# Performance work log

Hardware: AMD Instinct MI355X
Metric: run time of the kernel (lower is better)

## Reference

```python
import jax, jax.numpy as jnp
import numpy as np

TEMP = 0.07  # init temperature
EPS = 1e-12  # F.normalize eps


def _per_cloud_loss(fmap, labels):
    # fmap: [C, N] per-point features; labels: [N] int
    v = fmap.T  # [N, C]
    v = v / jnp.maximum(jnp.linalg.norm(v, axis=1, keepdims=True), EPS)
    # NxN similarity, exp then divide by temp (order matches original)
    dot = jnp.exp(v @ v.T) / TEMP  # [N, N]
    dot = dot - jnp.diag(jnp.diag(dot))  # zero the diagonal
    mask = (labels[:, None] == labels[None, :]).astype(dot.dtype)  # [N, N]
    mask_not = 1.0 - mask
    pos = (mask * dot).sum(1) / mask.sum(1)  # note: denom includes self, as in original
    neg = (mask_not * dot).sum(1) / mask_not.sum(1)
    return jnp.mean(-jnp.log(pos / (pos + neg)))


def setup_inputs() -> dict:
    key = jax.random.key(0)
    k1, k2 = jax.random.split(key)
    B, C, N = 8, 128, 4096
    features = jax.random.normal(k1, (B, C, N), dtype=jnp.float32)
    labels_all = jax.random.randint(k2, (B, N), 0, 16, dtype=jnp.int64)
    return {"features": features, "labels_all": labels_all}


def reference(features, labels_all):
    losses = jax.vmap(_per_cloud_loss)(features, labels_all)  # [B]
    return jnp.mean(losses)
```

## Files before the change

### kernel.cpp

```cpp
#include <hip/hip_runtime.h>
#include <stdint.h>

#define NPTS 4096
#define NC 128
#define NB 8
#define CSPLIT 8
#define COLS_PER (NPTS / CSPLIT)
#define TILES (COLS_PER / 64)
#define RPB 256

typedef __bf16 bf16x8 __attribute__((ext_vector_type(8)));
typedef float f32x4 __attribute__((ext_vector_type(4)));
typedef unsigned short u16;
typedef unsigned int u32;
typedef unsigned long long u64;

__device__ inline float fast_exp2(float x) { return __builtin_amdgcn_exp2f(x); }

__device__ inline u16 f2bf(float x) {
    u32 u = __float_as_uint(x);
    u32 r = (u + 0x7fffu + ((u >> 16) & 1u)) >> 16;
    return (u16)r;
}

typedef __attribute__((address_space(1))) const void glb_void;
typedef __attribute__((address_space(3))) void lds_void;
__device__ inline void gload_lds16(const void* g, void* l) {
    __builtin_amdgcn_global_load_lds((glb_void*)g, (lds_void*)l, 16, 0, 0);
}

__device__ inline bf16x8 scale8(bf16x8 v) {
#pragma unroll
    for (int k = 0; k < 8; ++k) v[k] = (__bf16)((float)v[k] * 1.44269504f);
    return v;
}

__global__ __launch_bounds__(256) void hist_kernel(const int* __restrict__ labels,
                                                   int* __restrict__ counts,
                                                   int* __restrict__ baseg,
                                                   u32* __restrict__ zb) {
    int b = blockIdx.x, tid = threadIdx.x;
    if (b == 0 && tid < 2) zb[tid] = 0u;
    __shared__ int cnt[64][16];
    __shared__ int tot[16];
    for (int i = tid; i < 64 * 16; i += 256) ((int*)cnt)[i] = 0;
    __syncthreads();
    for (int n = tid; n < NPTS; n += 256)
        atomicAdd(&cnt[n >> 6][labels[b * NPTS + n] & 15], 1);
    __syncthreads();
    if (tid < 16) {
        int s = 0;
        for (int k = 0; k < 64; ++k) s += cnt[k][tid];
        counts[b * 16 + tid] = s;
        tot[tid] = s;
    }
    __syncthreads();
    if (tid == 0) {
        int run = 0;
        for (int l = 0; l < 16; ++l) { int c = tot[l]; tot[l] = run; run += c; }
    }
    __syncthreads();
    if (tid < 16) {
        int run = tot[tid];
        for (int k = 0; k < 64; ++k) {
            baseg[(b * 64 + k) * 16 + tid] = run;
            run += cnt[k][tid];
        }
    }
}

__global__ __launch_bounds__(256) void norm_kernel(const float* __restrict__ feat,
                                                   const int* __restrict__ labels,
                                                   const int* __restrict__ baseg,
                                                   u16* __restrict__ vbf,
                                                   int* __restrict__ slab) {
    int b = blockIdx.y;
    int blk = blockIdx.x;
    int tid = threadIdx.x;
    int n0 = blk * 64;
    __shared__ float tile[64][129];
    __shared__ float part[8][64];
    __shared__ float rn[64];
    __shared__ int lpos[64];
    const float* fb = feat + (size_t)b * NC * NPTS;
    int nslot = tid & 31;
    int ty = tid >> 5;
    float s0 = 0.f, s1 = 0.f;
#pragma unroll
    for (int i = 0; i < 16; ++i) {
        int c = i * 8 + ty;
        float2 x = *(const float2*)(fb + (size_t)c * NPTS + n0 + 2 * nslot);
        tile[2 * nslot][c] = x.x;
        tile[2 * nslot + 1][c] = x.y;
        s0 += x.x * x.x;
        s1 += x.y * x.y;
    }
    part[ty][2 * nslot] = s0;
    part[ty][2 * nslot + 1] = s1;
    __syncthreads();
    if (tid < 64) {
        float s = 0.f;
#pragma unroll
        for (int t = 0; t < 8; ++t) s += part[t][tid];
        rn[tid] = 1.f / fmaxf(sqrtf(s), 1e-12f);
        int myl = labels[b * NPTS + n0 + tid] & 15;
        u64 mymask = 0ull;
#pragma unroll
        for (int L = 0; L < 16; ++L) {
            u64 bl = __ballot(myl == L);
            if (myl == L) mymask = bl;
        }
        int rank = __popcll(mymask & ((1ull << tid) - 1ull));
        int pos = baseg[(b * 64 + blk) * 16 + myl] + rank;
        lpos[tid] = pos;
        slab[b * NPTS + pos] = myl;
    }
    __syncthreads();
    u32* out = (u32*)vbf;
#pragma unroll
    for (int i = 0; i < 16; ++i) {
        int idx = tid + i * 256;
        int p = idx >> 6, k = idx & 63;
        float r = rn[p];
        float x0 = tile[p][2 * k] * r;
        float x1 = tile[p][2 * k + 1] * r;
        out[((size_t)b * NPTS + lpos[p]) * 64 + k] = (u32)f2bf(x0) | ((u32)f2bf(x1) << 16);
    }
}


#define META(S)                                                                   \
    const int rbase##S = row0 + wave * 64 + S * 16;                               \
    const int lrp##S = lab[rbase##S + myq] | (lab[rbase##S + myq + 1] << 8) |     \
                       (lab[rbase##S + myq + 2] << 16) |                          \
                       (lab[rbase##S + myq + 3] << 24);                           \
    const int slo##S = __builtin_amdgcn_readfirstlane(lab[rbase##S]);             \
    const int shi##S = __builtin_amdgcn_readfirstlane(lab[rbase##S + 15]);        \
    const bool suni##S = (slo##S == shi##S);                                      \
    const int key##S =                                                            \
        __builtin_amdgcn_readfirstlane((rbase##S & ~63) | ((rbase##S >> 4) & 3));

#define LDA(S)                                                                    \
    bf16x8 af##S##0, af##S##1, af##S##2, af##S##3;                                \
    {                                                                             \
        const u16* ap = vb + (size_t)(rbase##S + ln) * NC + quad * 8;             \
        af##S##0 = scale8(*(const bf16x8*)(ap));                                  \
        af##S##1 = scale8(*(const bf16x8*)(ap + 32));                             \
        af##S##2 = scale8(*(const bf16x8*)(ap + 64));                             \
        af##S##3 = scale8(*(const bf16x8*)(ap + 96));                             \
    }

#define ACC_MASK(S, L)                                                            \
    {                                                                             \
        bool m0 = (((lrp##S) & 255) == (L));                                      \
        bool m1 = ((((lrp##S) >> 8) & 255) == (L));                               \
        bool m2 = ((((lrp##S) >> 16) & 255) == (L));                              \
        bool m3 = ((((lrp##S) >> 24) & 255) == (L));                              \
        float e0 = fast_exp2(d[0]), e1 = fast_exp2(d[1]);                         \
        float e2 = fast_exp2(d[2]), e3 = fast_exp2(d[3]);                         \
        ps##S[0] += m0 ? e0 : 0.f; pn##S[0] += m0 ? 0.f : e0;                     \
        ps##S[1] += m1 ? e1 : 0.f; pn##S[1] += m1 ? 0.f : e1;                     \
        ps##S[2] += m2 ? e2 : 0.f; pn##S[2] += m2 ? 0.f : e2;                     \
        ps##S[3] += m3 ? e3 : 0.f; pn##S[3] += m3 ? 0.f : e3;                     \
    }

#define DO_S(S)                                                                   \
    {                                                                             \
        f32x4 d = {0.f, 0.f, 0.f, 0.f};                                           \
        d = __builtin_amdgcn_mfma_f32_16x16x32_bf16(af##S##0, bf0, d, 0, 0, 0);   \
        d = __builtin_amdgcn_mfma_f32_16x16x32_bf16(af##S##1, bf1, d, 0, 0, 0);   \
        d = __builtin_amdgcn_mfma_f32_16x16x32_bf16(af##S##2, bf2, d, 0, 0, 0);   \
        d = __builtin_amdgcn_mfma_f32_16x16x32_bf16(af##S##3, bf3, d, 0, 0, 0);   \
        if (key##S == ctsub) {         \
            int lc = clabs[cbase + ln];                                           \
            float e0 = fast_exp2(d[0]), e1 = fast_exp2(d[1]);                     \
            float e2 = fast_exp2(d[2]), e3 = fast_exp2(d[3]);                     \
            if (ln == myq + 0) e0 = 0.f;                                          \
            if (ln == myq + 1) e1 = 0.f;                                          \
            if (ln == myq + 2) e2 = 0.f;                                          \
            if (ln == myq + 3) e3 = 0.f;                                          \
            bool m0 = (((lrp##S) & 255) == lc);                                   \
            bool m1 = ((((lrp##S) >> 8) & 255) == lc);                            \
            bool m2 = ((((lrp##S) >> 16) & 255) == lc);                           \
            bool m3 = ((((lrp##S) >> 24) & 255) == lc);                           \
            ps##S[0] += m0 ? e0 : 0.f; pn##S[0] += m0 ? 0.f : e0;                 \
            ps##S[1] += m1 ? e1 : 0.f; pn##S[1] += m1 ? 0.f : e1;                 \
            ps##S[2] += m2 ? e2 : 0.f; pn##S[2] += m2 ? 0.f : e2;                 \
            ps##S[3] += m3 ? e3 : 0.f; pn##S[3] += m3 ? 0.f : e3;                 \
        } else if (cuni) {                           \
            if (clo < slo##S || clo > shi##S) {          \
                pn##S[0] += fast_exp2(d[0]); pn##S[1] += fast_exp2(d[1]);         \
                pn##S[2] += fast_exp2(d[2]); pn##S[3] += fast_exp2(d[3]);         \
            } else if (suni##S) {                        \
                ps##S[0] += fast_exp2(d[0]); ps##S[1] += fast_exp2(d[1]);         \
                ps##S[2] += fast_exp2(d[2]); ps##S[3] += fast_exp2(d[3]);         \
            } else {             \
                ACC_MASK(S, clo)                                                  \
            }                                                                     \
        } else {                                     \
            int lc2 = clabs[cbase + ln];                                          \
            ACC_MASK(S, lc2)                                                      \
        }                                                                         \
    }

#define STAGE(dst, tt)                                                            \
    gload_lds16(src + (tt) * 1024 + g40, (dst) + (wave * 4 + 0) * 512);           \
    gload_lds16(src + (tt) * 1024 + g41, (dst) + (wave * 4 + 1) * 512);           \
    gload_lds16(src + (tt) * 1024 + g42, (dst) + (wave * 4 + 2) * 512);           \
    gload_lds16(src + (tt) * 1024 + g43, (dst) + (wave * 4 + 3) * 512);

#define RED4(v)                                                                   \
    v[0] += __shfl_xor(v[0], off); v[1] += __shfl_xor(v[1], off);                 \
    v[2] += __shfl_xor(v[2], off); v[3] += __shfl_xor(v[3], off);

#define WR(S)                                                                     \
    {                                                                             \
        size_t o = ((size_t)cs * NB + b) * NPTS + rbase##S + myq;                 \
        float4 w0 = make_float4(ps##S[0], pn##S[0], ps##S[1], pn##S[1]);          \
        float4 w1 = make_float4(ps##S[2], pn##S[2], ps##S[3], pn##S[3]);          \
        *(float4*)(rowacc + 2 * o) = w0;                                          \
        *(float4*)(rowacc + 2 * o + 4) = w1;                                      \
    }

__global__ __launch_bounds__(256, 1) void sim_kernel(const u16* __restrict__ vbf,
                                                     const int* __restrict__ slab,
                                                     float* __restrict__ rowacc) {
    int bid = blockIdx.x;
    int rt = bid >> 6;
    int combo = bid & 63;
    int b = combo >> 3;
    int cs = combo & 7;
    int row0 = rt * RPB;
    int c0 = cs * COLS_PER;
    int tid = threadIdx.x;
    int wave = tid >> 6, lane = tid & 63;
    int quad = lane >> 4, ln = lane & 15;
    int myq = quad * 4;

    const u16* vb = vbf + (size_t)b * NPTS * NC;
    const int* lab = slab + b * NPTS;

    META(0) META(1) META(2) META(3)
    LDA(0) LDA(1) LDA(2) LDA(3)

    f32x4 ps0 = {0.f, 0.f, 0.f, 0.f}, ps1 = ps0, ps2 = ps0, ps3 = ps0;
    f32x4 pn0 = ps0, pn1 = ps0, pn2 = ps0, pn3 = ps0;

    __shared__ u16 cols[2][64 * 128];
    __shared__ int clabs[COLS_PER];
    clabs[tid] = lab[c0 + tid];
    clabs[tid + 256] = lab[c0 + 256 + tid];

    const uint4* src = (const uint4*)(vb + (size_t)c0 * NC);
    const int i160 = (wave * 4 + 0) * 64 + lane;
    const int i161 = (wave * 4 + 1) * 64 + lane;
    const int i162 = (wave * 4 + 2) * 64 + lane;
    const int i163 = (wave * 4 + 3) * 64 + lane;
    const int g40 = (i160 >> 4) * 16 + ((i160 & 15) ^ ((i160 >> 4) & 15));
    const int g41 = (i161 >> 4) * 16 + ((i161 & 15) ^ ((i161 >> 4) & 15));
    const int g42 = (i162 >> 4) * 16 + ((i162 & 15) ^ ((i162 >> 4) & 15));
    const int g43 = (i163 >> 4) * 16 + ((i163 & 15) ^ ((i163 >> 4) & 15));
    const int boff0 = ((0 * 4 + quad) ^ ln) * 8;
    const int boff1 = ((1 * 4 + quad) ^ ln) * 8;
    const int boff2 = ((2 * 4 + quad) ^ ln) * 8;
    const int boff3 = ((3 * 4 + quad) ^ ln) * 8;

    u16* bufA = &cols[0][0];
    u16* bufB = &cols[1][0];

    STAGE(bufA, 0)

    int ct = c0;
    for (int t = 0; t < TILES; ++t, ct += 64) {
        __syncthreads();
        if (t < TILES - 1) { STAGE(bufB, t + 1) }

#pragma unroll
        for (int sub = 0; sub < 4; ++sub) {
            const u16* rowb = bufA + (sub * 16 + ln) * 128;
            bf16x8 bf0 = *(const bf16x8*)(rowb + boff0);
            bf16x8 bf1 = *(const bf16x8*)(rowb + boff1);
            bf16x8 bf2 = *(const bf16x8*)(rowb + boff2);
            bf16x8 bf3 = *(const bf16x8*)(rowb + boff3);
            int cbase = t * 64 + sub * 16;
            int clo = __builtin_amdgcn_readfirstlane(clabs[cbase]);
            int chi = __builtin_amdgcn_readfirstlane(clabs[cbase + 15]);
            bool cuni = (clo == chi);
            int ctsub = ct | sub;
            DO_S(0) DO_S(1) DO_S(2) DO_S(3)
        }
        u16* tmp = bufA; bufA = bufB; bufB = tmp;
    }

#pragma unroll
    for (int off = 1; off < 16; off <<= 1) {
        RED4(ps0) RED4(pn0) RED4(ps1) RED4(pn1)
        RED4(ps2) RED4(pn2) RED4(ps3) RED4(pn3)
    }
    if (ln == 0) { WR(0) WR(1) WR(2) WR(3) }
}

__global__ __launch_bounds__(256) void loss_kernel(const float2* __restrict__ rowacc,
                                                   const int* __restrict__ slab,
                                                   const int* __restrict__ counts,
                                                   float* __restrict__ acc,
                                                   u32* __restrict__ ticket,
                                                   float* __restrict__ out) {
    int idx = blockIdx.x * 256 + threadIdx.x;
    int b = idx >> 12;
    float ps = 0.f, pn = 0.f;
#pragma unroll
    for (int cs = 0; cs < CSPLIT; ++cs) {
        float2 v = rowacc[(size_t)cs * NB * NPTS + idx];
        ps += v.x;
        pn += v.y;
    }
    int lb = slab[idx] & 15;
    int cnt = counts[b * 16 + lb];
    float p = ps / (float)cnt;
    float n = pn / (float)(NPTS - cnt);
    float loss = -__logf(p / (p + n));
#pragma unroll
    for (int off = 1; off < 64; off <<= 1) loss += __shfl_xor(loss, off);
    __shared__ float w[4];
    if ((threadIdx.x & 63) == 0) w[threadIdx.x >> 6] = loss;
    __syncthreads();
    if (threadIdx.x == 0) {
        atomicAdd(acc, w[0] + w[1] + w[2] + w[3]);
        __threadfence();
        u32 t = atomicAdd(ticket, 1u);
        if (t == gridDim.x - 1) {
            float v2 = atomicAdd(acc, 0.f);
            out[0] = v2 * (1.f / (float)(NB * NPTS));
        }
    }
}

extern "C" void kernel_launch(void* const* d_in, const int* in_sizes, int n_in,
                              void* d_out, int out_size, void* d_ws, size_t ws_size,
                              hipStream_t stream) {
    const float* feat = (const float*)d_in[0];
    const int* labels = (const int*)d_in[1];
    float* out = (float*)d_out;

    float* acc = (float*)d_ws;
    u32* ticket = (u32*)((char*)d_ws + 4);
    int* counts = (int*)((char*)d_ws + 256);
    int* baseg = (int*)((char*)d_ws + 1024);
    int* slab = (int*)((char*)d_ws + 36864);
    float* rowacc = (float*)((char*)d_ws + 172032);
    u16* vbf = (u16*)((char*)d_ws + 172032 + (size_t)CSPLIT * NB * NPTS * 8);

    hist_kernel<<<dim3(NB), 256, 0, stream>>>(labels, counts, baseg, (u32*)d_ws);
    norm_kernel<<<dim3(64, NB), 256, 0, stream>>>(feat, labels, baseg, vbf, slab);
    sim_kernel<<<dim3(16 * 64), 256, 0, stream>>>(vbf, slab, rowacc);
    loss_kernel<<<dim3(NB * NPTS / 256), 256, 0, stream>>>((const float2*)rowacc, slab, counts,
                                                           acc, ticket, out);
}
```

Baseline: 141.6 us.

## Load column fragments directly from global into registers, dropping LDS staging

Replaces the double-buffered LDS staging of 64-column tiles (global_load_lds plus per-tile barriers) with direct per-wave global loads of the 16-column B fragments into registers, software-prefetched one group ahead. The diagonal key is simplified to compare against the 16-column group start. This removes __syncthreads and LDS traffic from the loop but makes each wave fetch the column data independently through L1/L2, so global load volume rises fourfold and latency hiding relies on a single group of prefetch.

```diff
diff --git a/kernel.cpp b/kernel.cpp
--- a/kernel.cpp
+++ b/kernel.cpp
@@ -6,7 +6,7 @@
 #define NB 8
 #define CSPLIT 8
 #define COLS_PER (NPTS / CSPLIT)
-#define TILES (COLS_PER / 64)
+#define NGRP (COLS_PER / 16)
 #define RPB 256
 
 typedef __bf16 bf16x8 __attribute__((ext_vector_type(8)));
@@ -21,12 +21,6 @@
     u32 u = __float_as_uint(x);
     u32 r = (u + 0x7fffu + ((u >> 16) & 1u)) >> 16;
     return (u16)r;
-}
-
-typedef __attribute__((address_space(1))) const void glb_void;
-typedef __attribute__((address_space(3))) void lds_void;
-__device__ inline void gload_lds16(const void* g, void* l) {
-    __builtin_amdgcn_global_load_lds((glb_void*)g, (lds_void*)l, 16, 0, 0);
 }
 
 __device__ inline bf16x8 scale8(bf16x8 v) {
@@ -137,8 +131,7 @@
     const int slo##S = __builtin_amdgcn_readfirstlane(lab[rbase##S]);             \
     const int shi##S = __builtin_amdgcn_readfirstlane(lab[rbase##S + 15]);        \
     const bool suni##S = (slo##S == shi##S);                                      \
-    const int key##S =                                                            \
-        __builtin_amdgcn_readfirstlane((rbase##S & ~63) | ((rbase##S >> 4) & 3));
+    const int key##S = __builtin_amdgcn_readfirstlane(rbase##S);
 
 #define LDA(S)                                                                    \
     bf16x8 af##S##0, af##S##1, af##S##2, af##S##3;                                \
@@ -171,7 +164,7 @@
         d = __builtin_amdgcn_mfma_f32_16x16x32_bf16(af##S##1, bf1, d, 0, 0, 0);   \
         d = __builtin_amdgcn_mfma_f32_16x16x32_bf16(af##S##2, bf2, d, 0, 0, 0);   \
         d = __builtin_amdgcn_mfma_f32_16x16x32_bf16(af##S##3, bf3, d, 0, 0, 0);   \
-        if (key##S == ctsub) {         \
+        if (key##S == cg16) {    \
             int lc = clabs[cbase + ln];                                           \
             float e0 = fast_exp2(d[0]), e1 = fast_exp2(d[1]);                     \
             float e2 = fast_exp2(d[2]), e3 = fast_exp2(d[3]);                     \
@@ -187,7 +180,7 @@
             ps##S[1] += m1 ? e1 : 0.f; pn##S[1] += m1 ? 0.f : e1;                 \
             ps##S[2] += m2 ? e2 : 0.f; pn##S[2] += m2 ? 0.f : e2;                 \
             ps##S[3] += m3 ? e3 : 0.f; pn##S[3] += m3 ? 0.f : e3;                 \
-        } else if (cuni) {                           \
+        } else if (cuni) {                          \
             if (clo < slo##S || clo > shi##S) {          \
                 pn##S[0] += fast_exp2(d[0]); pn##S[1] += fast_exp2(d[1]);         \
                 pn##S[2] += fast_exp2(d[2]); pn##S[3] += fast_exp2(d[3]);         \
@@ -197,17 +190,28 @@
             } else {             \
                 ACC_MASK(S, clo)                                                  \
             }                                                                     \
-        } else {                                     \
+        } else {                                    \
             int lc2 = clabs[cbase + ln];                                          \
             ACC_MASK(S, lc2)                                                      \
         }                                                                         \
     }
 
-#define STAGE(dst, tt)                                                            \
-    gload_lds16(src + (tt) * 1024 + g40, (dst) + (wave * 4 + 0) * 512);           \
-    gload_lds16(src + (tt) * 1024 + g41, (dst) + (wave * 4 + 1) * 512);           \
-    gload_lds16(src + (tt) * 1024 + g42, (dst) + (wave * 4 + 2) * 512);           \
-    gload_lds16(src + (tt) * 1024 + g43, (dst) + (wave * 4 + 3) * 512);
+#define PREFETCH()                                                                \
+    nb0 = *(const bf16x8*)(bp);                                                   \
+    nb1 = *(const bf16x8*)(bp + 32);                                              \
+    nb2 = *(const bf16x8*)(bp + 64);                                              \
+    nb3 = *(const bf16x8*)(bp + 96);                                              \
+    bp += 16 * NC;
+
+#define COMPUTE(CG)                                                               \
+    {                                                                             \
+        const int cbase = (CG) * 16;                                              \
+        const int clo = __builtin_amdgcn_readfirstlane(clabs[cbase]);             \
+        const int chi = __builtin_amdgcn_readfirstlane(clabs[cbase + 15]);        \
+        const bool cuni = (clo == chi);                                           \
+        const int cg16 = c0 + cbase;                                              \
+        DO_S(0) DO_S(1) DO_S(2) DO_S(3)                                           \
+    }
 
 #define RED4(v)                                                                   \
     v[0] += __shfl_xor(v[0], off); v[1] += __shfl_xor(v[1], off);                 \
@@ -246,50 +250,23 @@
     f32x4 ps0 = {0.f, 0.f, 0.f, 0.f}, ps1 = ps0, ps2 = ps0, ps3 = ps0;
     f32x4 pn0 = ps0, pn1 = ps0, pn2 = ps0, pn3 = ps0;
 
-    __shared__ u16 cols[2][64 * 128];
     __shared__ int clabs[COLS_PER];
     clabs[tid] = lab[c0 + tid];
     clabs[tid + 256] = lab[c0 + 256 + tid];
-
-    const uint4* src = (const uint4*)(vb + (size_t)c0 * NC);
-    const int i160 = (wave * 4 + 0) * 64 + lane;
-    const int i161 = (wave * 4 + 1) * 64 + lane;
-    const int i162 = (wave * 4 + 2) * 64 + lane;
-    const int i163 = (wave * 4 + 3) * 64 + lane;
-    const int g40 = (i160 >> 4) * 16 + ((i160 & 15) ^ ((i160 >> 4) & 15));
-    const int g41 = (i161 >> 4) * 16 + ((i161 & 15) ^ ((i161 >> 4) & 15));
-    const int g42 = (i162 >> 4) * 16 + ((i162 & 15) ^ ((i162 >> 4) & 15));
-    const int g43 = (i163 >> 4) * 16 + ((i163 & 15) ^ ((i163 >> 4) & 15));
-    const int boff0 = ((0 * 4 + quad) ^ ln) * 8;
-    const int boff1 = ((1 * 4 + quad) ^ ln) * 8;
-    const int boff2 = ((2 * 4 + quad) ^ ln) * 8;
-    const int boff3 = ((3 * 4 + quad) ^ ln) * 8;
-
-    u16* bufA = &cols[0][0];
-    u16* bufB = &cols[1][0];
-
-    STAGE(bufA, 0)
-
-    int ct = c0;
-    for (int t = 0; t < TILES; ++t, ct += 64) {
-        __syncthreads();
-        if (t < TILES - 1) { STAGE(bufB, t + 1) }
-
-#pragma unroll
-        for (int sub = 0; sub < 4; ++sub) {
-            const u16* rowb = bufA + (sub * 16 + ln) * 128;
-            bf16x8 bf0 = *(const bf16x8*)(rowb + boff0);
-            bf16x8 bf1 = *(const bf16x8*)(rowb + boff1);
-            bf16x8 bf2 = *(const bf16x8*)(rowb + boff2);
-            bf16x8 bf3 = *(const bf16x8*)(rowb + boff3);
-            int cbase = t * 64 + sub * 16;
-            int clo = __builtin_amdgcn_readfirstlane(clabs[cbase]);
-            int chi = __builtin_amdgcn_readfirstlane(clabs[cbase + 15]);
-            bool cuni = (clo == chi);
-            int ctsub = ct | sub;
-            DO_S(0) DO_S(1) DO_S(2) DO_S(3)
-        }
-        u16* tmp = bufA; bufA = bufB; bufB = tmp;
+    __syncthreads();
+
+    const u16* bp = vb + (size_t)(c0 + ln) * NC + quad * 8;
+    bf16x8 nb0, nb1, nb2, nb3;
+    PREFETCH()
+
+    for (int cg = 0; cg < NGRP - 1; ++cg) {
+        bf16x8 bf0 = nb0, bf1 = nb1, bf2 = nb2, bf3 = nb3;
+        PREFETCH()
+        COMPUTE(cg)
+    }
+    {
+        bf16x8 bf0 = nb0, bf1 = nb1, bf2 = nb2, bf3 = nb3;
+        COMPUTE(NGRP - 1)
     }
 
 #pragma unroll
```

New measurement: 154.2 us. 1.09x slower.

## Exploit similarity matrix symmetry by computing only upper-triangular tile pairs

Applied to the files above, without the earlier changes.

The sim kernel now processes only the 136 upper-triangular 256x256 tile pairs per cloud instead of the full 16x16 grid. Each off-diagonal block accumulates both row sums and column sums, with column sums reduced through an LDS buffer and written to the transposed slice. This roughly halves the MFMA and exp work, but adds per-subtile shuffles, LDS read-modify-write, a larger rowacc buffer, and a 16-slice reduction in the loss kernel. Because each pair writes into a distinct slice, no atomics are needed.

```diff
diff --git a/kernel.cpp b/kernel.cpp
--- a/kernel.cpp
+++ b/kernel.cpp
@@ -4,10 +4,10 @@
 #define NPTS 4096
 #define NC 128
 #define NB 8
-#define CSPLIT 8
-#define COLS_PER (NPTS / CSPLIT)
-#define TILES (COLS_PER / 64)
-#define RPB 256
+#define NT 16
+#define NPAIR 136
+#define NSLICE 16
+#define TILES 4
 
 typedef __bf16 bf16x8 __attribute__((ext_vector_type(8)));
 typedef float f32x4 __attribute__((ext_vector_type(4)));
@@ -137,8 +137,7 @@
     const int slo##S = __builtin_amdgcn_readfirstlane(lab[rbase##S]);             \
     const int shi##S = __builtin_amdgcn_readfirstlane(lab[rbase##S + 15]);        \
     const bool suni##S = (slo##S == shi##S);                                      \
-    const int key##S =                                                            \
-        __builtin_amdgcn_readfirstlane((rbase##S & ~63) | ((rbase##S >> 4) & 3));
+    const int key##S = __builtin_amdgcn_readfirstlane(rbase##S);
 
 #define LDA(S)                                                                    \
     bf16x8 af##S##0, af##S##1, af##S##2, af##S##3;                                \
@@ -150,7 +149,7 @@
         af##S##3 = scale8(*(const bf16x8*)(ap + 96));                             \
     }
 
-#define ACC_MASK(S, L)                                                            \
+#define ACC_MASK_BOTH(S, L)                                                       \
     {                                                                             \
         bool m0 = (((lrp##S) & 255) == (L));                                      \
         bool m1 = ((((lrp##S) >> 8) & 255) == (L));                               \
@@ -162,6 +161,8 @@
         ps##S[1] += m1 ? e1 : 0.f; pn##S[1] += m1 ? 0.f : e1;                     \
         ps##S[2] += m2 ? e2 : 0.f; pn##S[2] += m2 ? 0.f : e2;                     \
         ps##S[3] += m3 ? e3 : 0.f; pn##S[3] += m3 ? 0.f : e3;                     \
+        pcs += (m0 ? e0 : 0.f) + (m1 ? e1 : 0.f) + (m2 ? e2 : 0.f) + (m3 ? e3 : 0.f); \
+        pcn += (m0 ? 0.f : e0) + (m1 ? 0.f : e1) + (m2 ? 0.f : e2) + (m3 ? 0.f : e3); \
     }
 
 #define DO_S(S)                                                                   \
@@ -171,7 +172,7 @@
         d = __builtin_amdgcn_mfma_f32_16x16x32_bf16(af##S##1, bf1, d, 0, 0, 0);   \
         d = __builtin_amdgcn_mfma_f32_16x16x32_bf16(af##S##2, bf2, d, 0, 0, 0);   \
         d = __builtin_amdgcn_mfma_f32_16x16x32_bf16(af##S##3, bf3, d, 0, 0, 0);   \
-        if (key##S == ctsub) {         \
+        if (key##S == cg16) {    \
             int lc = clabs[cbase + ln];                                           \
             float e0 = fast_exp2(d[0]), e1 = fast_exp2(d[1]);                     \
             float e2 = fast_exp2(d[2]), e3 = fast_exp2(d[3]);                     \
@@ -187,19 +188,23 @@
             ps##S[1] += m1 ? e1 : 0.f; pn##S[1] += m1 ? 0.f : e1;                 \
             ps##S[2] += m2 ? e2 : 0.f; pn##S[2] += m2 ? 0.f : e2;                 \
             ps##S[3] += m3 ? e3 : 0.f; pn##S[3] += m3 ? 0.f : e3;                 \
-        } else if (cuni) {                           \
-            if (clo < slo##S || clo > shi##S) {          \
-                pn##S[0] += fast_exp2(d[0]); pn##S[1] += fast_exp2(d[1]);         \
-                pn##S[2] += fast_exp2(d[2]); pn##S[3] += fast_exp2(d[3]);         \
-            } else if (suni##S) {                        \
-                ps##S[0] += fast_exp2(d[0]); ps##S[1] += fast_exp2(d[1]);         \
-                ps##S[2] += fast_exp2(d[2]); ps##S[3] += fast_exp2(d[3]);         \
+        } else if (cuni) {                          \
+            if (clo < slo##S || clo > shi##S) {                 \
+                float e0 = fast_exp2(d[0]), e1 = fast_exp2(d[1]);                 \
+                float e2 = fast_exp2(d[2]), e3 = fast_exp2(d[3]);                 \
+                pn##S[0] += e0; pn##S[1] += e1; pn##S[2] += e2; pn##S[3] += e3;   \
+                pcn += (e0 + e1) + (e2 + e3);                                     \
+            } else if (suni##S) {                               \
+                float e0 = fast_exp2(d[0]), e1 = fast_exp2(d[1]);                 \
+                float e2 = fast_exp2(d[2]), e3 = fast_exp2(d[3]);                 \
+                ps##S[0] += e0; ps##S[1] += e1; ps##S[2] += e2; ps##S[3] += e3;   \
+                pcs += (e0 + e1) + (e2 + e3);                                     \
             } else {             \
-                ACC_MASK(S, clo)                                                  \
+                ACC_MASK_BOTH(S, clo)                                             \
             }                                                                     \
-        } else {                                     \
+        } else {                                    \
             int lc2 = clabs[cbase + ln];                                          \
-            ACC_MASK(S, lc2)                                                      \
+            ACC_MASK_BOTH(S, lc2)                                                 \
         }                                                                         \
     }
 
@@ -215,7 +220,7 @@
 
 #define WR(S)                                                                     \
     {                                                                             \
-        size_t o = ((size_t)cs * NB + b) * NPTS + rbase##S + myq;                 \
+        size_t o = ((size_t)J * NB + b) * NPTS + rbase##S + myq;                  \
         float4 w0 = make_float4(ps##S[0], pn##S[0], ps##S[1], pn##S[1]);          \
         float4 w1 = make_float4(ps##S[2], pn##S[2], ps##S[3], pn##S[3]);          \
         *(float4*)(rowacc + 2 * o) = w0;                                          \
@@ -226,12 +231,18 @@
                                                      const int* __restrict__ slab,
                                                      float* __restrict__ rowacc) {
     int bid = blockIdx.x;
-    int rt = bid >> 6;
-    int combo = bid & 63;
-    int b = combo >> 3;
-    int cs = combo & 7;
-    int row0 = rt * RPB;
-    int c0 = cs * COLS_PER;
+    int b = bid & 7;
+    int p = bid >> 3;
+    int I = 0;
+    {
+        int rem = p;
+        while (rem >= NT - I) { rem -= NT - I; ++I; }
+        p = rem;
+    }
+    int J = I + p;
+    const bool isdiag = (I == J);
+    int row0 = I * 256;
+    int cbase0 = J * 256;
     int tid = threadIdx.x;
     int wave = tid >> 6, lane = tid & 63;
     int quad = lane >> 4, ln = lane & 15;
@@ -247,11 +258,13 @@
     f32x4 pn0 = ps0, pn1 = ps0, pn2 = ps0, pn3 = ps0;
 
     __shared__ u16 cols[2][64 * 128];
-    __shared__ int clabs[COLS_PER];
-    clabs[tid] = lab[c0 + tid];
-    clabs[tid + 256] = lab[c0 + 256 + tid];
-
-    const uint4* src = (const uint4*)(vb + (size_t)c0 * NC);
+    __shared__ int clabs[256];
+    __shared__ float2 clds[4][256];
+    clabs[tid] = lab[cbase0 + tid];
+#pragma unroll
+    for (int k = 0; k < 8; ++k) ((float*)clds)[tid + k * 256] = 0.f;
+
+    const uint4* src = (const uint4*)(vb + (size_t)cbase0 * NC);
     const int i160 = (wave * 4 + 0) * 64 + lane;
     const int i161 = (wave * 4 + 1) * 64 + lane;
     const int i162 = (wave * 4 + 2) * 64 + lane;
@@ -270,8 +283,7 @@
 
     STAGE(bufA, 0)
 
-    int ct = c0;
-    for (int t = 0; t < TILES; ++t, ct += 64) {
+    for (int t = 0; t < TILES; ++t) {
         __syncthreads();
         if (t < TILES - 1) { STAGE(bufB, t + 1) }
 
@@ -282,12 +294,20 @@
             bf16x8 bf1 = *(const bf16x8*)(rowb + boff1);
             bf16x8 bf2 = *(const bf16x8*)(rowb + boff2);
             bf16x8 bf3 = *(const bf16x8*)(rowb + boff3);
-            int cbase = t * 64 + sub * 16;
-            int clo = __builtin_amdgcn_readfirstlane(clabs[cbase]);
-            int chi = __builtin_amdgcn_readfirstlane(clabs[cbase + 15]);
-            bool cuni = (clo == chi);
-            int ctsub = ct | sub;
+            const int cbase = t * 64 + sub * 16;
+            const int clo = __builtin_amdgcn_readfirstlane(clabs[cbase]);
+            const int chi = __builtin_amdgcn_readfirstlane(clabs[cbase + 15]);
+            const bool cuni = (clo == chi);
+            const int cg16 = cbase0 + cbase;
+            float pcs = 0.f, pcn = 0.f;
             DO_S(0) DO_S(1) DO_S(2) DO_S(3)
+            pcs += __shfl_xor(pcs, 16); pcs += __shfl_xor(pcs, 32);
+            pcn += __shfl_xor(pcn, 16); pcn += __shfl_xor(pcn, 32);
+            if (!isdiag && quad == 0) {
+                float2 v = clds[wave][cbase + ln];
+                v.x += pcs; v.y += pcn;
+                clds[wave][cbase + ln] = v;
+            }
         }
         u16* tmp = bufA; bufA = bufB; bufB = tmp;
     }
@@ -298,6 +318,15 @@
         RED4(ps2) RED4(pn2) RED4(ps3) RED4(pn3)
     }
     if (ln == 0) { WR(0) WR(1) WR(2) WR(3) }
+
+    __syncthreads();
+    if (!isdiag) {
+        float2 a0 = clds[0][tid], a1 = clds[1][tid];
+        float2 a2 = clds[2][tid], a3 = clds[3][tid];
+        float cx = (a0.x + a1.x) + (a2.x + a3.x);
+        float cy = (a0.y + a1.y) + (a2.y + a3.y);
+        ((float2*)rowacc)[((size_t)I * NB + b) * NPTS + cbase0 + tid] = make_float2(cx, cy);
+    }
 }
 
 __global__ __launch_bounds__(256) void loss_kernel(const float2* __restrict__ rowacc,
@@ -310,8 +339,8 @@
     int b = idx >> 12;
     float ps = 0.f, pn = 0.f;
 #pragma unroll
-    for (int cs = 0; cs < CSPLIT; ++cs) {
-        float2 v = rowacc[(size_t)cs * NB * NPTS + idx];
+    for (int s = 0; s < NSLICE; ++s) {
+        float2 v = rowacc[(size_t)s * NB * NPTS + idx];
         ps += v.x;
         pn += v.y;
     }
@@ -349,11 +378,11 @@
     int* baseg = (int*)((char*)d_ws + 1024);
     int* slab = (int*)((char*)d_ws + 36864);
     float* rowacc = (float*)((char*)d_ws + 172032);
-    u16* vbf = (u16*)((char*)d_ws + 172032 + (size_t)CSPLIT * NB * NPTS * 8);
+    u16* vbf = (u16*)((char*)d_ws + 172032 + (size_t)NSLICE * NB * NPTS * 8);
 
     hist_kernel<<<dim3(NB), 256, 0, stream>>>(labels, counts, baseg, (u32*)d_ws);
     norm_kernel<<<dim3(64, NB), 256, 0, stream>>>(feat, labels, baseg, vbf, slab);
-    sim_kernel<<<dim3(16 * 64), 256, 0, stream>>>(vbf, slab, rowacc);
+    sim_kernel<<<dim3(NPAIR * NB), 256, 0, stream>>>(vbf, slab, rowacc);
     loss_kernel<<<dim3(NB * NPTS / 256), 256, 0, stream>>>((const float2*)rowacc, slab, counts,
                                                            acc, ticket, out);
 }
```

Result: faster. 138.5 us (-2.1%).
